# Kernel tuning notes

Hardware: AMD Instinct MI355X
Metric: run time of the kernel (lower is better)

The kernel has to match this reference:

```python
import math
import jax, jax.numpy as jnp
import numpy as np

B, S, D, H = 2, 2048, 1024, 16
DH = D // H


def setup_inputs() -> dict:
    key = jax.random.key(0)
    ks = jax.random.split(key, 6)
    scale = 1.0 / math.sqrt(D)  # xavier-ish scale for stability
    inp = {
        "query": jax.random.normal(ks[0], (B, S, D), jnp.float32),
        "mask": jax.random.randint(ks[1], (B, S, S), 0, 2) > 0,
        "Wq": jax.random.normal(ks[2], (D, D), jnp.float32) * scale,
        "bq": jnp.zeros((D,), jnp.float32),
        "Wk": jax.random.normal(ks[3], (D, D), jnp.float32) * scale,
        "bk": jnp.zeros((D,), jnp.float32),
        "Wv": jax.random.normal(ks[4], (D, D), jnp.float32) * scale,
        "bv": jnp.zeros((D,), jnp.float32),
        "Wo": jax.random.normal(ks[5], (D, D), jnp.float32) * scale,
        "bo": jnp.zeros((D,), jnp.float32),
    }
    return inp


def reference(query, mask, Wq, bq, Wk, bk, Wv, bv, Wo, bo):
    # self-attention: memory = query
    def shape(x):  # [B,S,D] -> [B,H,S,DH]
        return x.reshape(B, S, H, DH).transpose(0, 2, 1, 3)

    q = shape(query @ Wq.T + bq) / math.sqrt(DH)
    k = shape(query @ Wk.T + bk)
    v = shape(query @ Wv.T + bv)
    scores = jnp.einsum("bhqd,bhkd->bhqk", q, k)
    scores = jnp.where(mask[:, None, :, :], jnp.float32(-1e18), scores)
    attn = jax.nn.softmax(scores, axis=-1)
    # dropout is identity in eval mode
    ctx = jnp.einsum("bhqk,bhkd->bhqd", attn, v)
    ctx = ctx.transpose(0, 2, 1, 3).reshape(B, S, D)
    return ctx @ Wo.T + bo
```

## Files before the change

### kernel.cpp

```cpp
#include <hip/hip_runtime.h>

#define B_ 2
#define S_ 2048
#define D_ 1024
#define H_ 16
#define DH_ 64

typedef float f32x4 __attribute__((ext_vector_type(4)));
typedef short s16x8 __attribute__((ext_vector_type(8)));
typedef __bf16 bf16x8 __attribute__((ext_vector_type(8)));
typedef unsigned int uint;

template <typename T>
static __device__ auto mfma_sel(T a, T b, f32x4 c, int)
    -> decltype(__builtin_amdgcn_mfma_f32_16x16x32_bf16(a, b, c, 0, 0, 0)) {
  return __builtin_amdgcn_mfma_f32_16x16x32_bf16(a, b, c, 0, 0, 0);
}
template <typename T>
static __device__ f32x4 mfma_sel(T a, T b, f32x4 c, long) {
  return __builtin_amdgcn_mfma_f32_16x16x32_bf16(
      __builtin_bit_cast(bf16x8, a), __builtin_bit_cast(bf16x8, b), c, 0, 0, 0);
}
static __device__ __forceinline__ f32x4 mfma_bf16(s16x8 a, s16x8 b, f32x4 c) {
  return mfma_sel(a, b, c, 0);
}

static __device__ __forceinline__ short f2bf(float f) {
  unsigned u = __float_as_uint(f);
  u += 0x7fffu + ((u >> 16) & 1u);
  return (short)(u >> 16);
}

static __device__ __forceinline__ short f2bf_rn(float f) {
  return __builtin_bit_cast(short, (__bf16)f);
}

static __device__ __forceinline__ void async16(const short* g, short* l) {
  __builtin_amdgcn_global_load_lds(
      (const __attribute__((address_space(1))) unsigned int*)g,
      (__attribute__((address_space(3))) unsigned int*)l, 16, 0, 0);
}

__global__ void detect_mask_kernel(const uint* __restrict__ m,
                                   int* __restrict__ flag) {
  int lane = threadIdx.x;
  bool gt1 = false, notf = false;
  for (int i = 0; i < 16; ++i) {
    uint v = m[lane * 16 + i];
    if (v > 1u) gt1 = true;
    if (v != 0u && v != 0x3F800000u) notf = true;
  }
  unsigned long long b1 = __ballot(gt1);
  unsigned long long b2 = __ballot(notf);
  if (lane == 0) {
    int f;
    if (b1 == 0ull) f = 1;
    else if (b2 == 0ull) f = 2;
    else f = 0;
    *flag = f;
  }
}

__global__ __launch_bounds__(256) void build_bitmask_kernel(
    const void* __restrict__ mask, const int* __restrict__ flag,
    uint* __restrict__ bmT) {
  int w = blockIdx.x * 256 + threadIdx.x;
  int b = w >> 17;
  int rem = w & 131071;
  int q = rem >> 6;
  int kt = rem & 63;
  int mty = *flag;
  uint bits = 0;
  if (mty == 0) {
    const uint* p = (const uint*)((const unsigned char*)mask +
                                  ((size_t)b * S_ + q) * S_ + (size_t)kt * 32);
#pragma unroll
    for (int i = 0; i < 8; ++i) {
      uint v = p[i];
#pragma unroll
      for (int j = 0; j < 4; ++j)
        if ((v >> (8 * j)) & 0xffu) bits |= 1u << (i * 4 + j);
    }
  } else {
    const uint* p = (const uint*)mask + ((size_t)b * S_ + q) * S_ + kt * 32;
#pragma unroll
    for (int i = 0; i < 32; ++i)
      if (p[i]) bits |= 1u << i;
  }
  bmT[((size_t)b * (S_ / 32) + kt) * S_ + q] = bits;
}

__global__ __launch_bounds__(256) void convert_kernel(
    const float* __restrict__ q, const float* __restrict__ wq,
    const float* __restrict__ wk, const float* __restrict__ wv,
    short* __restrict__ qbf, short* __restrict__ wqkv) {
  int bid = blockIdx.x;
  int t = threadIdx.x;
  const float* src;
  short* dst;
  int rowbase, seg;
  if (bid < 2048)      { src = q;  dst = qbf;  rowbase = bid * 2;          seg = -1; }
  else if (bid < 2560) { src = wq; dst = wqkv; rowbase = (bid - 2048) * 2; seg = 0; }
  else if (bid < 3072) { src = wk; dst = wqkv; rowbase = (bid - 2560) * 2; seg = 1; }
  else                 { src = wv; dst = wqkv; rowbase = (bid - 3072) * 2; seg = 2; }
  int rl = rowbase + (t >> 7);
  int k = (t & 127) * 8;
  const float* s8 = src + (size_t)rl * 1024 + k;
  f32x4 a = *(const f32x4*)s8;
  f32x4 b = *(const f32x4*)(s8 + 4);
  s16x8 r;
  r[0] = f2bf(a[0]); r[1] = f2bf(a[1]); r[2] = f2bf(a[2]); r[3] = f2bf(a[3]);
  r[4] = f2bf(b[0]); r[5] = f2bf(b[1]); r[6] = f2bf(b[2]); r[7] = f2bf(b[3]);
  int grow = (seg < 0) ? rl : (seg * 1024 + rl);
  size_t chunk = ((size_t)(grow >> 4) * 32 + (k >> 5)) * 64 +
                 ((k >> 3) & 3) * 16 + (grow & 15);
  *(s16x8*)(dst + chunk * 8) = r;
}

__global__ __launch_bounds__(256) void convert_wo_kernel(
    const float* __restrict__ wo, short* __restrict__ wob) {
  size_t i = ((size_t)blockIdx.x * 256 + threadIdx.x) * 8;
  f32x4 a = *(const f32x4*)(wo + i);
  f32x4 b = *(const f32x4*)(wo + i + 4);
  s16x8 r;
  r[0] = f2bf(a[0]); r[1] = f2bf(a[1]); r[2] = f2bf(a[2]); r[3] = f2bf(a[3]);
  r[4] = f2bf(b[0]); r[5] = f2bf(b[1]); r[6] = f2bf(b[2]); r[7] = f2bf(b[3]);
  *(s16x8*)(wob + i) = r;
}

__global__ __launch_bounds__(256) void gemm_qkv_kernel(
    const short* __restrict__ A, const short* __restrict__ Bt,
    const float* __restrict__ bq, const float* __restrict__ bk,
    const float* __restrict__ bv, short* __restrict__ q_ws,
    short* __restrict__ KF, short* __restrict__ VF) {
  __shared__ short lds[8192];
  const int tid = threadIdx.x;
  const int lane = tid & 63;
  const int wave = tid >> 6;
  const int l16 = lane & 15;
  const int quad = lane >> 4;
  const int mb0 = blockIdx.x * 8;
  const int nb0 = blockIdx.y * 8;
  const int m0 = blockIdx.x * 128 + (wave >> 1) * 64;
  const int n0 = blockIdx.y * 128 + (wave & 1) * 64;
  const int g = tid >> 6, c = tid & 63;

  f32x4 acc[4][4];
#pragma unroll
  for (int i = 0; i < 4; ++i)
#pragma unroll
    for (int j = 0; j < 4; ++j) acc[i][j] = (f32x4){0.f, 0.f, 0.f, 0.f};

  for (int kb = 0; kb < 32; ++kb) {
    async16(A + (((size_t)(mb0 + g) * 32 + kb) * 64 + c) * 8, lds + tid * 8);
    async16(A + (((size_t)(mb0 + g + 4) * 32 + kb) * 64 + c) * 8,
            lds + 2048 + tid * 8);
    async16(Bt + (((size_t)(nb0 + g) * 32 + kb) * 64 + c) * 8,
            lds + 4096 + tid * 8);
    async16(Bt + (((size_t)(nb0 + g + 4) * 32 + kb) * 64 + c) * 8,
            lds + 6144 + tid * 8);
    __syncthreads();
    s16x8 a[4], b[4];
#pragma unroll
    for (int i = 0; i < 4; ++i)
      a[i] = *(const s16x8*)(lds + (((wave >> 1) * 4 + i) * 64 + lane) * 8);
#pragma unroll
    for (int j = 0; j < 4; ++j)
      b[j] = *(const s16x8*)(lds + 4096 + (((wave & 1) * 4 + j) * 64 + lane) * 8);
#pragma unroll
    for (int i = 0; i < 4; ++i)
#pragma unroll
      for (int j = 0; j < 4; ++j) acc[i][j] = mfma_bf16(a[i], b[j], acc[i][j]);
    __syncthreads();
  }

#pragma unroll
  for (int i = 0; i < 4; ++i) {
#pragma unroll
    for (int j = 0; j < 4; ++j) {
#pragma unroll
      for (int r = 0; r < 4; ++r) {
        int m = m0 + i * 16 + quad * 4 + r;
        int n = n0 + j * 16 + l16;
        int seg = n >> 10, nl = n & 1023;
        float bias = (seg == 0) ? bq[nl] : ((seg == 1) ? bk[nl] : bv[nl]);
        float v = acc[i][j][r] + bias;
        if (seg == 0) v *= 0.18033688011112042f;
        int bb = m >> 11, s = m & (S_ - 1);
        int hh = nl >> 6, dh = nl & 63;
        int bh = bb * H_ + hh;
        short bv16 = f2bf(v);
        if (seg == 0) {
          q_ws[((size_t)bh * S_ + s) * DH_ + dh] = bv16;
        } else if (seg == 1) {
          int kt = s >> 5, r5 = s & 31;
          int kkb = r5 >> 4, kl16 = r5 & 15;
          int kf = dh >> 5, qd = (dh >> 3) & 3, e = dh & 7;
          KF[(size_t)bh * 131072 +
             ((size_t)kt * 256 + (kkb * 2 + kf) * 64 + qd * 16 + kl16) * 8 + e] = bv16;
        } else {
          int kt = s >> 5, ko = s & 31;
          int hi = ko >> 4, qd = (ko >> 2) & 3, j4 = ko & 3;
          int nb = dh >> 4, vl16 = dh & 15, e = hi * 4 + j4;
          VF[(size_t)bh * 131072 +
             ((size_t)kt * 256 + nb * 64 + qd * 16 + vl16) * 8 + e] = bv16;
        }
      }
    }
  }
}

__global__ __launch_bounds__(512, 4) void attn_kernel(
    const short* __restrict__ Q, const short* __restrict__ KF,
    const short* __restrict__ VF, const uint* __restrict__ bmT,
    short* __restrict__ ctx_out) {
  __shared__ float fl[8704];
  const int tid = threadIdx.x;
  const int lane = tid & 63;
  const int wave = tid >> 6;
  const int qw = wave >> 1;
  const int kbt = wave & 1;
  const int l16 = lane & 15;
  const int quad = lane >> 4;
  const int xcd = blockIdx.x & 7;
  const int slot = blockIdx.x >> 3;
  const int bh = xcd * 4 + (slot >> 4);
  const int qt128 = slot & 15;
  const int b = bh >> 4;
  const int h = bh & 15;
  const int qbase = qt128 * 128 + qw * 32;

  const short* Qh = Q + (size_t)bh * S_ * DH_;
  const short* Kh = KF + (size_t)bh * 131072 + kbt * 2048 + lane * 8;
  const short* Vh = VF + (size_t)bh * 131072 + kbt * 2048 + lane * 8;
  const uint* bmb = bmT + (size_t)b * (S_ / 32) * S_;

  s16x8 qf[2][2];
#pragma unroll
  for (int qg = 0; qg < 2; ++qg)
#pragma unroll
    for (int kf = 0; kf < 2; ++kf)
      qf[qg][kf] = *(const s16x8*)(Qh + (size_t)(qbase + qg * 16 + l16) * DH_ +
                                   kf * 32 + quad * 8);

  f32x4 ctx[2][4];
#pragma unroll
  for (int qg = 0; qg < 2; ++qg)
#pragma unroll
    for (int nb = 0; nb < 4; ++nb) ctx[qg][nb] = (f32x4){0.f, 0.f, 0.f, 0.f};
  float ls[2] = {0.f, 0.f};

  uint wc0 = bmb[(size_t)kbt * S_ + qbase + l16];
  uint wc1 = bmb[(size_t)kbt * S_ + qbase + 16 + l16];
  uint wn0 = bmb[(size_t)(2 + kbt) * S_ + qbase + l16];
  uint wn1 = bmb[(size_t)(2 + kbt) * S_ + qbase + 16 + l16];

  s16x8 kaA[2][2], kaB[2][2];
#pragma unroll
  for (int kb = 0; kb < 2; ++kb)
#pragma unroll
    for (int kf = 0; kf < 2; ++kf)
      kaA[kb][kf] = *(const s16x8*)(Kh + (kb * 2 + kf) * 512);

#define ATTN_TILE(KC, KN, T, PREF)                                            \
  {                                                                           \
    if (PREF) {                                                               \
      const short* kp = Kh + (size_t)((T) + 1) * 4096;                        \
      _Pragma("unroll") for (int kb = 0; kb < 2; ++kb)                        \
          _Pragma("unroll") for (int kf = 0; kf < 2; ++kf)                    \
              KN[kb][kf] = *(const s16x8*)(kp + (kb * 2 + kf) * 512);         \
    }                                                                         \
    uint a0 = 0, a1 = 0;                                                      \
    if ((T) + 2 < 32) {                                                       \
      a0 = bmb[(size_t)(2 * (T) + 4 + kbt) * S_ + qbase + l16];               \
      a1 = bmb[(size_t)(2 * (T) + 4 + kbt) * S_ + qbase + 16 + l16];          \
    }                                                                         \
    const short* vp = Vh + (size_t)(T) * 4096;                                \
    s16x8 vb[4];                                                              \
    _Pragma("unroll") for (int nb = 0; nb < 4; ++nb)                          \
        vb[nb] = *(const s16x8*)(vp + nb * 512);                              \
    s16x8 pa[2];                                                              \
    const uint wsh0 = wc0 >> (quad * 4);                                      \
    const uint wsh1 = wc1 >> (quad * 4);                                      \
    _Pragma("unroll") for (int qg = 0; qg < 2; ++qg) {                        \
      f32x4 sc[2];                                                            \
      _Pragma("unroll") for (int kb = 0; kb < 2; ++kb) {                      \
        f32x4 t0 =                                                            \
            mfma_bf16(KC[kb][0], qf[qg][0], (f32x4){0.f, 0.f, 0.f, 0.f});     \
        sc[kb] = mfma_bf16(KC[kb][1], qf[qg][1], t0);                         \
      }                                                                       \
      const uint wsh = qg ? wsh1 : wsh0;                                      \
      float sum = 0.f;                                                        \
      _Pragma("unroll") for (int kb = 0; kb < 2; ++kb)                        \
          _Pragma("unroll") for (int r = 0; r < 4; ++r) {                     \
        int bit = (wsh >> (kb * 16 + r)) & 1;                                 \
        float p = bit ? 0.f : __builtin_amdgcn_exp2f(sc[kb][r]);              \
        sum += p;                                                             \
        pa[qg][kb * 4 + r] = f2bf_rn(p);                                      \
      }                                                                       \
      ls[qg] += sum;                                                          \
    }                                                                         \
    _Pragma("unroll") for (int nb = 0; nb < 4; ++nb)                          \
        _Pragma("unroll") for (int qg = 0; qg < 2; ++qg)                      \
            ctx[qg][nb] = mfma_bf16(pa[qg], vb[nb], ctx[qg][nb]);             \
    wc0 = wn0;                                                                \
    wc1 = wn1;                                                                \
    wn0 = a0;                                                                 \
    wn1 = a1;                                                                 \
  }

  for (int t2 = 0; t2 < 16; ++t2) {
    ATTN_TILE(kaA, kaB, 2 * t2, 1)
    ATTN_TILE(kaB, kaA, 2 * t2 + 1, (t2 < 15))
  }
#undef ATTN_TILE

  const int foff = qw * 2176;
  if (kbt) {
#pragma unroll
    for (int qg = 0; qg < 2; ++qg) {
#pragma unroll
      for (int nb = 0; nb < 4; ++nb)
#pragma unroll
        for (int r = 0; r < 4; ++r)
          fl[foff + ((qg * 4 + nb) * 4 + r) * 64 + lane] = ctx[qg][nb][r];
      fl[foff + 2048 + qg * 64 + lane] = ls[qg];
    }
  }
  __syncthreads();
  if (!kbt) {
#pragma unroll
    for (int qg = 0; qg < 2; ++qg) {
#pragma unroll
      for (int nb = 0; nb < 4; ++nb)
#pragma unroll
        for (int r = 0; r < 4; ++r)
          ctx[qg][nb][r] += fl[foff + ((qg * 4 + nb) * 4 + r) * 64 + lane];
      ls[qg] += fl[foff + 2048 + qg * 64 + lane];
      ls[qg] += __shfl_xor(ls[qg], 16);
      ls[qg] += __shfl_xor(ls[qg], 32);
    }

#pragma unroll
    for (int qg = 0; qg < 2; ++qg)
#pragma unroll
      for (int r = 0; r < 4; ++r) {
        float lr = __shfl(ls[qg], quad * 4 + r);
        float inv = 1.f / lr;
        int srow = qbase + qg * 16 + quad * 4 + r;
#pragma unroll
        for (int nb = 0; nb < 4; ++nb) {
          int col = h * DH_ + nb * 16 + l16;
          ctx_out[(size_t)(b * S_ + srow) * D_ + col] = f2bf(ctx[qg][nb][r] * inv);
        }
      }
  }
}

__global__ __launch_bounds__(256) void gemm_final_kernel(
    const short* __restrict__ A, const short* __restrict__ Bt,
    const float* __restrict__ bias, float* __restrict__ out) {
  __shared__ short lds[8192];
  const int tid = threadIdx.x;
  const int lane = tid & 63;
  const int wave = tid >> 6;
  const int l16 = lane & 15;
  const int quad = lane >> 4;
  const int m0 = blockIdx.x * 128;
  const int n0 = blockIdx.y * 128;
  const int g = tid >> 6, c = tid & 63;
  const int r15 = c & 15, qd = c >> 4;

  f32x4 acc[4][4];
#pragma unroll
  for (int i = 0; i < 4; ++i)
#pragma unroll
    for (int j = 0; j < 4; ++j) acc[i][j] = (f32x4){0.f, 0.f, 0.f, 0.f};

  for (int k0 = 0; k0 < 1024; k0 += 32) {
    async16(A + (size_t)(m0 + g * 16 + r15) * 1024 + k0 + qd * 8, lds + tid * 8);
    async16(A + (size_t)(m0 + (g + 4) * 16 + r15) * 1024 + k0 + qd * 8,
            lds + 2048 + tid * 8);
    async16(Bt + (size_t)(n0 + g * 16 + r15) * 1024 + k0 + qd * 8,
            lds + 4096 + tid * 8);
    async16(Bt + (size_t)(n0 + (g + 4) * 16 + r15) * 1024 + k0 + qd * 8,
            lds + 6144 + tid * 8);
    __syncthreads();
    s16x8 a[4], b[4];
#pragma unroll
    for (int i = 0; i < 4; ++i)
      a[i] = *(const s16x8*)(lds + (((wave >> 1) * 4 + i) * 64 + lane) * 8);
#pragma unroll
    for (int j = 0; j < 4; ++j)
      b[j] = *(const s16x8*)(lds + 4096 + (((wave & 1) * 4 + j) * 64 + lane) * 8);
#pragma unroll
    for (int i = 0; i < 4; ++i)
#pragma unroll
      for (int j = 0; j < 4; ++j) acc[i][j] = mfma_bf16(a[i], b[j], acc[i][j]);
    __syncthreads();
  }

  const int mw = m0 + (wave >> 1) * 64;
  const int nw = n0 + (wave & 1) * 64;
#pragma unroll
  for (int i = 0; i < 4; ++i)
#pragma unroll
    for (int j = 0; j < 4; ++j)
#pragma unroll
      for (int r = 0; r < 4; ++r) {
        int m = mw + i * 16 + quad * 4 + r;
        int n = nw + j * 16 + l16;
        out[(size_t)m * 1024 + n] = acc[i][j][r] + bias[n];
      }
}

extern "C" void kernel_launch(void* const* d_in, const int* in_sizes, int n_in,
                              void* d_out, int out_size, void* d_ws,
                              size_t ws_size, hipStream_t stream) {
  const float* query = (const float*)d_in[0];
  const void* mask = d_in[1];
  const float* Wq = (const float*)d_in[2];
  const float* bq = (const float*)d_in[3];
  const float* Wk = (const float*)d_in[4];
  const float* bk = (const float*)d_in[5];
  const float* Wv = (const float*)d_in[6];
  const float* bv = (const float*)d_in[7];
  const float* Wo = (const float*)d_in[8];
  const float* bo = (const float*)d_in[9];

  const size_t NE = (size_t)B_ * S_ * D_;
  short* ws_s = (short*)d_ws;
  short* q_ws = ws_s;
  short* KF = ws_s + NE;
  short* VF = ws_s + 2 * NE;
  short* ctx_ws = ws_s + 3 * NE;
  short* wo_bf = ws_s;
  short* qbf = (short*)d_out;
  short* wqkv = qbf + NE;
  uint* bmT = (uint*)(wqkv + 3145728);
  int* flag = (int*)(bmT + 262144);

  detect_mask_kernel<<<1, 64, 0, stream>>>((const uint*)mask, flag);
  build_bitmask_kernel<<<1024, 256, 0, stream>>>(mask, flag, bmT);
  convert_kernel<<<3584, 256, 0, stream>>>(query, Wq, Wk, Wv, qbf, wqkv);

  gemm_qkv_kernel<<<dim3(32, 24), 256, 0, stream>>>(qbf, wqkv, bq, bk, bv,
                                                    q_ws, KF, VF);

  attn_kernel<<<512, 512, 0, stream>>>(q_ws, KF, VF, bmT, ctx_ws);

  convert_wo_kernel<<<512, 256, 0, stream>>>(Wo, wo_bf);

  gemm_final_kernel<<<dim3(32, 8), 256, 0, stream>>>(ctx_ws, wo_bf, bo,
                                                     (float*)d_out);
}
```

Baseline: 238.6 us.

## Fuse prep kernels and compute softmax row sums with MFMA

```diff
diff --git a/kernel.cpp b/kernel.cpp
--- a/kernel.cpp
+++ b/kernel.cpp
@@ -41,39 +41,64 @@
       (__attribute__((address_space(3))) unsigned int*)l, 16, 0, 0);
 }
 
-__global__ void detect_mask_kernel(const uint* __restrict__ m,
-                                   int* __restrict__ flag) {
-  int lane = threadIdx.x;
-  bool gt1 = false, notf = false;
-  for (int i = 0; i < 16; ++i) {
-    uint v = m[lane * 16 + i];
-    if (v > 1u) gt1 = true;
-    if (v != 0u && v != 0x3F800000u) notf = true;
-  }
-  unsigned long long b1 = __ballot(gt1);
-  unsigned long long b2 = __ballot(notf);
-  if (lane == 0) {
-    int f;
-    if (b1 == 0ull) f = 1;
-    else if (b2 == 0ull) f = 2;
-    else f = 0;
-    *flag = f;
-  }
-}
-
-__global__ __launch_bounds__(256) void build_bitmask_kernel(
-    const void* __restrict__ mask, const int* __restrict__ flag,
-    uint* __restrict__ bmT) {
-  int w = blockIdx.x * 256 + threadIdx.x;
+__global__ __launch_bounds__(256) void prep_kernel(
+    const float* __restrict__ q, const float* __restrict__ wq,
+    const float* __restrict__ wk, const float* __restrict__ wv,
+    const void* __restrict__ mask, short* __restrict__ qbf,
+    short* __restrict__ wqkv, uint* __restrict__ bmT) {
+  __shared__ int s_gt1, s_notf;
+  const int bid = blockIdx.x;
+  const int t = threadIdx.x;
+
+  if (bid < 3584) {
+    const float* src;
+    short* dst;
+    int rowbase, seg;
+    if (bid < 2048)      { src = q;  dst = qbf;  rowbase = bid * 2;          seg = -1; }
+    else if (bid < 2560) { src = wq; dst = wqkv; rowbase = (bid - 2048) * 2; seg = 0; }
+    else if (bid < 3072) { src = wk; dst = wqkv; rowbase = (bid - 2560) * 2; seg = 1; }
+    else                 { src = wv; dst = wqkv; rowbase = (bid - 3072) * 2; seg = 2; }
+    int rl = rowbase + (t >> 7);
+    int k = (t & 127) * 8;
+    const float* s8 = src + (size_t)rl * 1024 + k;
+    f32x4 a = *(const f32x4*)s8;
+    f32x4 b = *(const f32x4*)(s8 + 4);
+    s16x8 r;
+    r[0] = f2bf(a[0]); r[1] = f2bf(a[1]); r[2] = f2bf(a[2]); r[3] = f2bf(a[3]);
+    r[4] = f2bf(b[0]); r[5] = f2bf(b[1]); r[6] = f2bf(b[2]); r[7] = f2bf(b[3]);
+    int grow = (seg < 0) ? rl : (seg * 1024 + rl);
+    size_t chunk = ((size_t)(grow >> 4) * 32 + (k >> 5)) * 64 +
+                   ((k >> 3) & 3) * 16 + (grow & 15);
+    *(s16x8*)(dst + chunk * 8) = r;
+    return;
+  }
+
+  if (t == 0) { s_gt1 = 0; s_notf = 0; }
+  __syncthreads();
+  {
+    const uint* m = (const uint*)mask;
+    bool gt1 = false, notf = false;
+#pragma unroll
+    for (int i = 0; i < 4; ++i) {
+      uint v = m[t * 4 + i];
+      if (v > 1u) gt1 = true;
+      if (v != 0u && v != 0x3F800000u) notf = true;
+    }
+    if (gt1) atomicOr(&s_gt1, 1);
+    if (notf) atomicOr(&s_notf, 1);
+  }
+  __syncthreads();
+  const int mty = s_gt1 ? (s_notf ? 0 : 2) : 1;
+
+  int w = (bid - 3584) * 256 + t;
   int b = w >> 17;
   int rem = w & 131071;
-  int q = rem >> 6;
+  int qq = rem >> 6;
   int kt = rem & 63;
-  int mty = *flag;
   uint bits = 0;
   if (mty == 0) {
     const uint* p = (const uint*)((const unsigned char*)mask +
-                                  ((size_t)b * S_ + q) * S_ + (size_t)kt * 32);
+                                  ((size_t)b * S_ + qq) * S_ + (size_t)kt * 32);
 #pragma unroll
     for (int i = 0; i < 8; ++i) {
       uint v = p[i];
@@ -82,39 +107,12 @@
         if ((v >> (8 * j)) & 0xffu) bits |= 1u << (i * 4 + j);
     }
   } else {
-    const uint* p = (const uint*)mask + ((size_t)b * S_ + q) * S_ + kt * 32;
+    const uint* p = (const uint*)mask + ((size_t)b * S_ + qq) * S_ + kt * 32;
 #pragma unroll
     for (int i = 0; i < 32; ++i)
       if (p[i]) bits |= 1u << i;
   }
-  bmT[((size_t)b * (S_ / 32) + kt) * S_ + q] = bits;
-}
-
-__global__ __launch_bounds__(256) void convert_kernel(
-    const float* __restrict__ q, const float* __restrict__ wq,
-    const float* __restrict__ wk, const float* __restrict__ wv,
-    short* __restrict__ qbf, short* __restrict__ wqkv) {
-  int bid = blockIdx.x;
-  int t = threadIdx.x;
-  const float* src;
-  short* dst;
-  int rowbase, seg;
-  if (bid < 2048)      { src = q;  dst = qbf;  rowbase = bid * 2;          seg = -1; }
-  else if (bid < 2560) { src = wq; dst = wqkv; rowbase = (bid - 2048) * 2; seg = 0; }
-  else if (bid < 3072) { src = wk; dst = wqkv; rowbase = (bid - 2560) * 2; seg = 1; }
-  else                 { src = wv; dst = wqkv; rowbase = (bid - 3072) * 2; seg = 2; }
-  int rl = rowbase + (t >> 7);
-  int k = (t & 127) * 8;
-  const float* s8 = src + (size_t)rl * 1024 + k;
-  f32x4 a = *(const f32x4*)s8;
-  f32x4 b = *(const f32x4*)(s8 + 4);
-  s16x8 r;
-  r[0] = f2bf(a[0]); r[1] = f2bf(a[1]); r[2] = f2bf(a[2]); r[3] = f2bf(a[3]);
-  r[4] = f2bf(b[0]); r[5] = f2bf(b[1]); r[6] = f2bf(b[2]); r[7] = f2bf(b[3]);
-  int grow = (seg < 0) ? rl : (seg * 1024 + rl);
-  size_t chunk = ((size_t)(grow >> 4) * 32 + (k >> 5)) * 64 +
-                 ((k >> 3) & 3) * 16 + (grow & 15);
-  *(s16x8*)(dst + chunk * 8) = r;
+  bmT[((size_t)b * (S_ / 32) + kt) * S_ + qq] = bits;
 }
 
 __global__ __launch_bounds__(256) void convert_wo_kernel(
@@ -214,7 +212,7 @@
     const short* __restrict__ Q, const short* __restrict__ KF,
     const short* __restrict__ VF, const uint* __restrict__ bmT,
     short* __restrict__ ctx_out) {
-  __shared__ float fl[8704];
+  __shared__ float fl[10240];
   const int tid = threadIdx.x;
   const int lane = tid & 63;
   const int wave = tid >> 6;
@@ -235,6 +233,9 @@
   const short* Vh = VF + (size_t)bh * 131072 + kbt * 2048 + lane * 8;
   const uint* bmb = bmT + (size_t)b * (S_ / 32) * S_;
 
+  const s16x8 onesv = {0x3F80, 0x3F80, 0x3F80, 0x3F80,
+                       0x3F80, 0x3F80, 0x3F80, 0x3F80};
+
   s16x8 qf[2][2];
 #pragma unroll
   for (int qg = 0; qg < 2; ++qg)
@@ -244,11 +245,13 @@
                                    kf * 32 + quad * 8);
 
   f32x4 ctx[2][4];
-#pragma unroll
-  for (int qg = 0; qg < 2; ++qg)
+  f32x4 lsf[2];
+#pragma unroll
+  for (int qg = 0; qg < 2; ++qg) {
 #pragma unroll
     for (int nb = 0; nb < 4; ++nb) ctx[qg][nb] = (f32x4){0.f, 0.f, 0.f, 0.f};
-  float ls[2] = {0.f, 0.f};
+    lsf[qg] = (f32x4){0.f, 0.f, 0.f, 0.f};
+  }
 
   uint wc0 = bmb[(size_t)kbt * S_ + qbase + l16];
   uint wc1 = bmb[(size_t)kbt * S_ + qbase + 16 + l16];
@@ -279,6 +282,7 @@
     s16x8 vb[4];                                                              \
     _Pragma("unroll") for (int nb = 0; nb < 4; ++nb)                          \
         vb[nb] = *(const s16x8*)(vp + nb * 512);                              \
+    __builtin_amdgcn_s_setprio(1);                                            \
     s16x8 pa[2];                                                              \
     const uint wsh0 = wc0 >> (quad * 4);                                      \
     const uint wsh1 = wc1 >> (quad * 4);                                      \
@@ -290,19 +294,19 @@
         sc[kb] = mfma_bf16(KC[kb][1], qf[qg][1], t0);                         \
       }                                                                       \
       const uint wsh = qg ? wsh1 : wsh0;                                      \
-      float sum = 0.f;                                                        \
       _Pragma("unroll") for (int kb = 0; kb < 2; ++kb)                        \
           _Pragma("unroll") for (int r = 0; r < 4; ++r) {                     \
         int bit = (wsh >> (kb * 16 + r)) & 1;                                 \
         float p = bit ? 0.f : __builtin_amdgcn_exp2f(sc[kb][r]);              \
-        sum += p;                                                             \
         pa[qg][kb * 4 + r] = f2bf_rn(p);                                      \
       }                                                                       \
-      ls[qg] += sum;                                                          \
     }                                                                         \
+    lsf[0] = mfma_bf16(pa[0], onesv, lsf[0]);                                 \
+    lsf[1] = mfma_bf16(pa[1], onesv, lsf[1]);                                 \
     _Pragma("unroll") for (int nb = 0; nb < 4; ++nb)                          \
         _Pragma("unroll") for (int qg = 0; qg < 2; ++qg)                      \
             ctx[qg][nb] = mfma_bf16(pa[qg], vb[nb], ctx[qg][nb]);             \
+    __builtin_amdgcn_s_setprio(0);                                            \
     wc0 = wn0;                                                                \
     wc1 = wn1;                                                                \
     wn0 = a0;                                                                 \
@@ -315,7 +319,7 @@
   }
 #undef ATTN_TILE
 
-  const int foff = qw * 2176;
+  const int foff = qw * 2560;
   if (kbt) {
 #pragma unroll
     for (int qg = 0; qg < 2; ++qg) {
@@ -324,7 +328,9 @@
 #pragma unroll
         for (int r = 0; r < 4; ++r)
           fl[foff + ((qg * 4 + nb) * 4 + r) * 64 + lane] = ctx[qg][nb][r];
-      fl[foff + 2048 + qg * 64 + lane] = ls[qg];
+#pragma unroll
+      for (int r = 0; r < 4; ++r)
+        fl[foff + 2048 + (qg * 4 + r) * 64 + lane] = lsf[qg][r];
     }
   }
   __syncthreads();
@@ -336,17 +342,16 @@
 #pragma unroll
         for (int r = 0; r < 4; ++r)
           ctx[qg][nb][r] += fl[foff + ((qg * 4 + nb) * 4 + r) * 64 + lane];
-      ls[qg] += fl[foff + 2048 + qg * 64 + lane];
-      ls[qg] += __shfl_xor(ls[qg], 16);
-      ls[qg] += __shfl_xor(ls[qg], 32);
+#pragma unroll
+      for (int r = 0; r < 4; ++r)
+        lsf[qg][r] += fl[foff + 2048 + (qg * 4 + r) * 64 + lane];
     }
 
 #pragma unroll
     for (int qg = 0; qg < 2; ++qg)
 #pragma unroll
       for (int r = 0; r < 4; ++r) {
-        float lr = __shfl(ls[qg], quad * 4 + r);
-        float inv = 1.f / lr;
+        float inv = 1.f / lsf[qg][r];
         int srow = qbase + qg * 16 + quad * 4 + r;
 #pragma unroll
         for (int nb = 0; nb < 4; ++nb) {
@@ -438,11 +443,9 @@
   short* qbf = (short*)d_out;
   short* wqkv = qbf + NE;
   uint* bmT = (uint*)(wqkv + 3145728);
-  int* flag = (int*)(bmT + 262144);
-
-  detect_mask_kernel<<<1, 64, 0, stream>>>((const uint*)mask, flag);
-  build_bitmask_kernel<<<1024, 256, 0, stream>>>(mask, flag, bmT);
-  convert_kernel<<<3584, 256, 0, stream>>>(query, Wq, Wk, Wv, qbf, wqkv);
+
+  prep_kernel<<<4608, 256, 0, stream>>>(query, Wq, Wk, Wv, mask, qbf, wqkv,
+                                        bmT);
 
   gemm_qkv_kernel<<<dim3(32, 24), 256, 0, stream>>>(qbf, wqkv, bq, bk, bv,
                                                     q_ws, KF, VF);
```

New measurement: 302.7 us. +26.9%, slower.
